# Performance work log

Measured on AMD Instinct MI355X. Metric: run time of the kernel, lower is better.

Reference implementation:

```python
import jax, jax.numpy as jnp
import numpy as np

_ICO_FACES0 = [
    [0,11,5],[0,5,1],[0,1,7],[0,7,10],[0,10,11],
    [1,5,9],[5,11,4],[11,10,2],[10,7,6],[7,1,8],
    [3,9,4],[3,4,2],[3,2,6],[3,6,8],[3,8,9],
    [4,9,5],[2,4,11],[6,2,10],[8,6,7],[9,8,1]]


def ico_sphere_np(level=1):
    t = (1.0 + 5.0 ** 0.5) / 2.0
    verts = np.array([[-1,t,0],[1,t,0],[-1,-t,0],[1,-t,0],
                      [0,-1,t],[0,1,t],[0,-1,-t],[0,1,-t],
                      [t,0,-1],[t,0,1],[-t,0,-1],[-t,0,1]], dtype=np.float64)
    verts = verts / np.linalg.norm(verts, axis=1, keepdims=True)
    faces = [list(f) for f in _ICO_FACES0]
    for _ in range(level):
        vlist = [v for v in verts]
        cache = {}
        def mid(a, b):
            k = (min(a, b), max(a, b))
            if k not in cache:
                v = vlist[a] + vlist[b]
                vlist.append(v / np.linalg.norm(v))
                cache[k] = len(vlist) - 1
            return cache[k]
        nf = []
        for a, b, c in faces:
            ab, bc, ca = mid(a, b), mid(b, c), mid(c, a)
            nf += [[a, ab, ca], [b, bc, ab], [c, ca, bc], [ab, bc, ca]]
        faces = nf
        verts = np.stack(vlist)
    return verts.astype(np.float32), np.array(faces, dtype=np.int32)


def make_template():
    verts, faces = ico_sphere_np(1)          # (42,3), (80,3)
    v = verts[None]                          # (1,42,3)
    vmin = v.min(axis=1, keepdims=True)
    vmax = v.max(axis=1, keepdims=True)
    center = (vmin + vmax) / 2.0
    scale = (vmax - vmin).max() / 2.0        # normalize_to_box
    tv = 1.4 * (v - center) / scale          # cage_size = 1.4
    return jnp.asarray(np.transpose(tv, (0, 2, 1))), jnp.asarray(faces)  # (1,3,42),(80,3)


def optimize_cage(cage, shape, distance=0.4, iters=100, step=0.01):
    # cage (1,3,C), shape (B,3,N)
    B = shape.shape[0]
    cage = jnp.broadcast_to(cage, (B,) + cage.shape[1:])
    def body(_, c):
        d = jnp.sqrt(jnp.sum((c[:, :, :, None] - shape[:, :, None, :]) ** 2, axis=1))  # (B,C,N)
        min_d = jnp.min(d, axis=2)                                                     # (B,C)
        upd = (min_d > distance).astype(c.dtype)
        return c + step * (-c) * upd[:, None, :]
    return jax.lax.fori_loop(0, iters, body, cage)


def mean_value_coordinates_3D(query, vertices, faces):
    # query (B,P,3), vertices (B,C,3), faces (F,3) shared across batch
    B, P, _ = query.shape
    C = vertices.shape[1]
    r1 = jnp.array([1, 2, 0]); r2 = jnp.array([2, 0, 1])
    uj = vertices[:, None] - query[:, :, None]            # (B,P,C,3)
    dj = jnp.linalg.norm(uj, axis=-1, keepdims=True)      # (B,P,C,1)
    uj = uj / dj
    ui = uj[:, :, faces]                                  # (B,P,F,3,3)
    li = jnp.linalg.norm(ui[:, :, :, r1] - ui[:, :, :, r2], axis=-1)  # (B,P,F,3)
    eps = 2e-5
    li = jnp.where(li >= 2, li - jax.lax.stop_gradient(li - (2 - eps)), li)
    li = jnp.where(li <= -2, li - jax.lax.stop_gradient(li + (2 - eps)), li)
    theta = 2.0 * jnp.arcsin(li / 2.0)                    # (B,P,F,3)
    h = jnp.sum(theta, axis=-1, keepdims=True) / 2.0      # (B,P,F,1)
    ci = 2.0 * jnp.sin(h) * jnp.sin(h - theta) / (jnp.sin(theta[..., r1]) * jnp.sin(theta[..., r2])) - 1.0
    ci = jnp.clip(ci, -1 + 1e-5, 1 - 1e-5)
    si = jnp.sign(jnp.linalg.det(ui))[..., None] * jnp.sqrt(1.0 - ci ** 2)  # (B,P,F,3)
    di = dj[..., 0][:, :, faces]                          # (B,P,F,3)
    wi = (theta - ci[..., r1] * theta[..., r2] - ci[..., r2] * theta[..., r1]) / (di * jnp.sin(theta[..., r1]) * si[..., r2])
    inside = (jnp.pi - h[..., 0]) < 1e-4                  # (B,P,F)
    any_inside = jnp.any(inside, axis=-1, keepdims=True)[..., None]  # (B,P,1,1)
    wi = jnp.where(any_inside, 0.0, wi)
    wi = jnp.where(inside[..., None], jnp.sin(theta) * di[..., r2] * di[..., r1], wi)
    # scatter face corners -> vertices (B,P,F*3) -> (B,P,C)
    wj = jnp.zeros((B, P, C), wi.dtype).at[:, :, faces.reshape(-1)].add(wi.reshape(B, P, -1))
    close = dj[..., 0] < 1e-8                             # (B,P,C)
    wj = jnp.where(jnp.any(close, axis=-1, keepdims=True), 0.0, wj)
    wj = jnp.where(close, 1.0, wj)
    sumWj = jnp.sum(wj, axis=-1, keepdims=True)
    sumWj = jnp.where(sumWj == 0, 1.0, sumWj)
    return wj / sumWj, wi


def setup_inputs() -> dict:
    key = jax.random.key(0)
    ks = jax.random.split(key, 12)
    B, N, FEAT = 16, 8192, 256
    template_vertices, faces = make_template()
    def lin(k, fi, fo):
        k1, k2 = jax.random.split(k)
        return (jax.random.normal(k1, (fi, fo), jnp.float32) / np.sqrt(fi).astype(np.float32),
                jax.random.normal(k2, (fo,), jnp.float32) * 0.01)
    W1, b1 = lin(ks[0], 2 * FEAT, 512)
    W2, b2 = lin(ks[1], 512, 512)
    W3, b3 = lin(ks[2], 512, 256)
    W4, b4 = lin(ks[3], 256, 42 * 3)
    return {
        'source_shape': jax.random.normal(ks[4], (B, 3, N), jnp.float32),
        'target_shape': jax.random.normal(ks[5], (B, 3, N), jnp.float32),
        'source_f': jax.random.normal(ks[6], (B, FEAT), jnp.float32),
        'target_f': jax.random.normal(ks[7], (B, FEAT), jnp.float32),
        'template_vertices': template_vertices, 'faces': faces,
        'W1': W1, 'b1': b1, 'W2': W2, 'b2': b2, 'W3': W3, 'b3': b3, 'W4': W4, 'b4': b4,
    }


def reference(source_shape, target_shape, source_f, target_f, template_vertices, faces,
              W1, b1, W2, b2, W3, b3, W4, b4):
    B = source_shape.shape[0]
    cage = optimize_cage(template_vertices, source_shape)        # (B,3,42)
    feat = jnp.concatenate([source_f, target_f], axis=-1)        # (B,512)
    h = jax.nn.relu(feat @ W1 + b1)
    h = jax.nn.relu(h @ W2 + b2)
    h = jax.nn.relu(h @ W3 + b3)
    influence_offset = h @ W4 + b4                               # (B,126)
    cage_offset = influence_offset.reshape(B, 3, -1)             # (B,3,42)
    new_cage = cage + cage_offset
    cage_t = jnp.transpose(cage, (0, 2, 1))                      # (B,42,3)
    new_cage_t = jnp.transpose(new_cage, (0, 2, 1))
    weights, _ = mean_value_coordinates_3D(jnp.transpose(source_shape, (0, 2, 1)), cage_t, faces)
    weights = jax.lax.stop_gradient(weights)                     # weights.detach() in deform_with_MVC
    deformed = jnp.einsum('bpc,bcd->bpd', weights, new_cage_t)   # (B,N,3)
    return cage_t, new_cage_t, jnp.transpose(deformed, (0, 2, 1)), weights, influence_offset
```

## Files before the change

kernel.cpp:

```cpp
#include <hip/hip_runtime.h>
#include <math.h>

#define BB 16
#define NP 8192
#define NV 42
#define NF 80
#define FEAT 256
#define PPB 64
#define FH  40

__device__ __forceinline__ float rcp_f(float x)  { return __builtin_amdgcn_rcpf(x); }
__device__ __forceinline__ float rsq_f(float x)  { return __builtin_amdgcn_rsqf(x); }
__device__ __forceinline__ float sqrt_f(float x) { return __builtin_amdgcn_sqrtf(x); }

__device__ __forceinline__ float theta_from_x(float x) {
  bool big = x > 0.5f;
  float z = big ? fmaf(-0.5f, x, 0.5f) : x * x;
  float s = big ? sqrt_f(z) : x;
  float P = fmaf(z, 0.022371875f, 0.030381944f);
  P = fmaf(z, P, 0.044642857f);
  P = fmaf(z, P, 0.075f);
  P = fmaf(z, P, 0.16666667f);
  float r = fmaf(s * z, P, s);
  return big ? fmaf(-4.f, r, 3.14159265358979f) : 2.f * r;
}

__global__ __launch_bounds__(256) void cage_opt_kernel(
    const float* __restrict__ tmpl,
    const float* __restrict__ src,
    float* __restrict__ cage)
{
  __shared__ float red[8];
  int b = blockIdx.x / NV;
  int v = blockIdx.x % NV;
  const float* sp = src + (size_t)b * 3 * NP;
  float cx = tmpl[v], cy = tmpl[NV + v], cz = tmpl[2 * NV + v];
  int k = 0;
  while (true) {
    float m = 3.4e38f;
    for (int i = threadIdx.x; i < NP; i += 256) {
      float dx = __fsub_rn(cx, sp[i]);
      float dy = __fsub_rn(cy, sp[NP + i]);
      float dz = __fsub_rn(cz, sp[2 * NP + i]);
      float ss = __fadd_rn(__fadd_rn(__fmul_rn(dx, dx), __fmul_rn(dy, dy)),
                           __fmul_rn(dz, dz));
      m = fminf(m, ss);
    }
    #pragma unroll
    for (int off = 32; off > 0; off >>= 1)
      m = fminf(m, __shfl_down(m, off, 64));
    int wid = threadIdx.x >> 6;
    __syncthreads();
    if ((threadIdx.x & 63) == 0) red[wid] = m;
    __syncthreads();
    if (threadIdx.x == 0) {
      float mm = fminf(fminf(red[0], red[1]), fminf(red[2], red[3]));
      red[4] = sqrtf(mm);
    }
    __syncthreads();
    float mind = red[4];
    if (mind > 0.4f && k < 100) {
      cx = __fsub_rn(cx, __fmul_rn(0.01f, cx));
      cy = __fsub_rn(cy, __fmul_rn(0.01f, cy));
      cz = __fsub_rn(cz, __fmul_rn(0.01f, cz));
      k++;
    } else {
      break;
    }
  }
  if (threadIdx.x == 0) {
    cage[(size_t)b * 3 * NV + v]          = cx;
    cage[(size_t)b * 3 * NV + NV + v]     = cy;
    cage[(size_t)b * 3 * NV + 2 * NV + v] = cz;
  }
}

__global__ __launch_bounds__(256) void linear_splitk(
    const float* __restrict__ in0, const float* __restrict__ in1,
    const float* __restrict__ W, const float* __restrict__ bias,
    float* __restrict__ out, int FI, int FO, int relu)
{
  __shared__ float sIn[512];
  __shared__ float part[4][64];
  int bb = blockIdx.y;
  int tid = threadIdx.x;
  for (int i = tid; i < FI; i += 256) {
    float v;
    if (in1) v = (i < FEAT) ? in0[(size_t)bb * FEAT + i]
                            : in1[(size_t)bb * FEAT + i - FEAT];
    else     v = in0[(size_t)bb * FI + i];
    sIn[i] = v;
  }
  __syncthreads();
  int o = blockIdx.x * 64 + (tid & 63);
  int kk = tid >> 6;
  int seg = FI >> 2;
  float acc = 0.f;
  const float* wp = W + o;
  #pragma unroll 4
  for (int i = kk * seg; i < (kk + 1) * seg; i++)
    acc = fmaf(sIn[i], wp[(size_t)i * FO], acc);
  part[kk][tid & 63] = acc;
  __syncthreads();
  if (tid < 64) {
    float r = ((part[0][tid] + part[1][tid]) + (part[2][tid] + part[3][tid]))
              + bias[o];
    out[(size_t)bb * FO + o] = relu ? fmaxf(r, 0.f) : r;
  }
}

__global__ __launch_bounds__(128) void l4_finalize_kernel(
    const float* __restrict__ h3,
    const float* __restrict__ W4, const float* __restrict__ b4,
    const float* __restrict__ cage,
    float* __restrict__ out_io,
    float* __restrict__ cage_t,
    float* __restrict__ ncage_t)
{
  __shared__ float sIn[256];
  int bb = blockIdx.x;
  int tid = threadIdx.x;
  sIn[tid] = h3[(size_t)bb * 256 + tid];
  sIn[tid + 128] = h3[(size_t)bb * 256 + tid + 128];
  __syncthreads();
  if (tid < 126) {
    float acc = b4[tid];
    const float* wp = W4 + tid;
    #pragma unroll 4
    for (int i = 0; i < 256; i++) acc = fmaf(sIn[i], wp[(size_t)i * 126], acc);
    out_io[(size_t)bb * 126 + tid] = acc;
    float c  = cage[(size_t)bb * 126 + tid];
    float nc = c + acc;
    int d = tid / NV, v = tid - d * NV;
    cage_t[(size_t)bb * NV * 3 + v * 3 + d]  = c;
    ncage_t[(size_t)bb * NV * 3 + v * 3 + d] = nc;
  }
}

__global__ __launch_bounds__(128, 3) void mvc_kernel(
    const float* __restrict__ src,
    const float* __restrict__ cage_t,
    const float* __restrict__ ncage_t,
    const int* __restrict__ faces,
    float* __restrict__ out_def,
    float* __restrict__ out_w)
{
  __shared__ float4 vpos[NV];
  __shared__ float4 npos[NV];
  __shared__ int fidp[NF];
  __shared__ float wj[2 * NV][PPB];
  __shared__ unsigned long long closeM[2][PPB];
  __shared__ int insideF[2][PPB];

  const float PI_F = 3.14159265358979323846f;
  int tid = threadIdx.x;
  int p   = tid & (PPB - 1);
  int hf  = tid >> 6;
  int b    = blockIdx.x / (NP / PPB);
  int pblk = blockIdx.x % (NP / PPB);
  int gp   = pblk * PPB + p;

  if (tid < NV) {
    const float* cp = cage_t + (size_t)b * NV * 3 + tid * 3;
    vpos[tid] = make_float4(cp[0], cp[1], cp[2], 0.f);
    const float* np_ = ncage_t + (size_t)b * NV * 3 + tid * 3;
    npos[tid] = make_float4(np_[0], np_[1], np_[2], 0.f);
  }
  if (tid < NF) {
    int f0 = faces[3 * tid], f1 = faces[3 * tid + 1], f2 = faces[3 * tid + 2];
    fidp[tid] = f0 | (f1 << 6) | (f2 << 12);
  }
  #pragma unroll
  for (int c = 0; c < NV; c++) wj[hf * NV + c][p] = 0.f;
  __syncthreads();

  float qx = src[(size_t)b * 3 * NP + gp];
  float qy = src[(size_t)b * 3 * NP + NP + gp];
  float qz = src[(size_t)b * 3 * NP + 2 * NP + gp];

  int anyInside = 0;
  unsigned long long closeMask = 0ull;

  auto face_geom = [&](int i, int& f0, int& f1, int& f2,
                       float& d0, float& d1, float& d2,
                       float& th0, float& th1, float& th2,
                       float& st0, float& st1, float& st2,
                       float& hh, float& sh, float& sm0, float& sm1, float& sm2,
                       float& sg) {
    int pk = fidp[i];
    f0 = pk & 63; f1 = (pk >> 6) & 63; f2 = pk >> 12;
    float4 v0 = vpos[f0], v1 = vpos[f1], v2 = vpos[f2];
    float a0x = v0.x - qx, a0y = v0.y - qy, a0z = v0.z - qz;
    float a1x = v1.x - qx, a1y = v1.y - qy, a1z = v1.z - qz;
    float a2x = v2.x - qx, a2y = v2.y - qy, a2z = v2.z - qz;
    float ss0 = fmaf(a0x, a0x, fmaf(a0y, a0y, a0z * a0z));
    float ss1 = fmaf(a1x, a1x, fmaf(a1y, a1y, a1z * a1z));
    float ss2 = fmaf(a2x, a2x, fmaf(a2y, a2y, a2z * a2z));
    float i0 = rsq_f(ss0), i1 = rsq_f(ss1), i2 = rsq_f(ss2);
    d0 = ss0 * i0; d1 = ss1 * i1; d2 = ss2 * i2;
    if (d0 < 1e-8f) closeMask |= (1ull << f0);
    if (d1 < 1e-8f) closeMask |= (1ull << f1);
    if (d2 < 1e-8f) closeMask |= (1ull << f2);
    float u0x = a0x * i0, u0y = a0y * i0, u0z = a0z * i0;
    float u1x = a1x * i1, u1y = a1y * i1, u1z = a1z * i1;
    float u2x = a2x * i2, u2y = a2y * i2, u2z = a2z * i2;
    float ex, ey, ez;
    ex = u1x - u2x; ey = u1y - u2y; ez = u1z - u2z;
    float x0 = 0.5f * sqrt_f(fmaf(ex, ex, fmaf(ey, ey, ez * ez)));
    ex = u2x - u0x; ey = u2y - u0y; ez = u2z - u0z;
    float x1 = 0.5f * sqrt_f(fmaf(ex, ex, fmaf(ey, ey, ez * ez)));
    ex = u0x - u1x; ey = u0y - u1y; ez = u0z - u1z;
    float x2 = 0.5f * sqrt_f(fmaf(ex, ex, fmaf(ey, ey, ez * ez)));
    if (x0 >= 1.f) x0 = 0.99999f;
    if (x1 >= 1.f) x1 = 0.99999f;
    if (x2 >= 1.f) x2 = 0.99999f;
    float cx0 = sqrt_f(fmaxf(fmaf(-x0, x0, 1.f), 0.f));
    float cx1 = sqrt_f(fmaxf(fmaf(-x1, x1, 1.f), 0.f));
    float cx2 = sqrt_f(fmaxf(fmaf(-x2, x2, 1.f), 0.f));
    th0 = theta_from_x(x0);
    th1 = theta_from_x(x1);
    th2 = theta_from_x(x2);
    hh  = 0.5f * ((th0 + th1) + th2);
    st0 = 2.f * (x0 * cx0);
    st1 = 2.f * (x1 * cx1);
    st2 = 2.f * (x2 * cx2);
    float A1 = x0 * (cx1 * cx2);
    float A2 = x1 * (cx0 * cx2);
    float A3 = x2 * (cx0 * cx1);
    float A4 = x0 * (x1 * x2);
    sh  = ((A1 + A2) + A3) - A4;
    sm0 = ((-A1 + A2) + A3) + A4;
    sm1 = ((A1 - A2) + A3) + A4;
    sm2 = ((A1 + A2) - A3) + A4;
    float det = u0x * fmaf(u1y, u2z, -u1z * u2y)
              - u0y * fmaf(u1x, u2z, -u1z * u2x)
              + u0z * fmaf(u1x, u2y, -u1y * u2x);
    sg = (det > 0.f) ? 1.f : ((det < 0.f) ? -1.f : 0.f);
  };

  #pragma unroll 1
  for (int i = hf * FH; i < hf * FH + FH; i++) {
    int f0, f1, f2;
    float d0, d1, d2, th0, th1, th2, st0, st1, st2, hh, sh, sm0, sm1, sm2, sg;
    face_geom(i, f0, f1, f2, d0, d1, d2, th0, th1, th2, st0, st1, st2,
              hh, sh, sm0, sm1, sm2, sg);
    if (PI_F - hh < 1e-4f) anyInside = 1;
    float twosh = 2.f * sh;
    float c0 = fmaf(twosh * sm0, rcp_f(st1 * st2), -1.f);
    float c1 = fmaf(twosh * sm1, rcp_f(st2 * st0), -1.f);
    float c2 = fmaf(twosh * sm2, rcp_f(st0 * st1), -1.f);
    c0 = fminf(fmaxf(c0, -0.99999f), 0.99999f);
    c1 = fminf(fmaxf(c1, -0.99999f), 0.99999f);
    c2 = fminf(fmaxf(c2, -0.99999f), 0.99999f);
    float s0 = sg * sqrt_f(fmaf(-c0, c0, 1.f));
    float s1 = sg * sqrt_f(fmaf(-c1, c1, 1.f));
    float s2 = sg * sqrt_f(fmaf(-c2, c2, 1.f));
    float w0 = (fmaf(-c2, th1, fmaf(-c1, th2, th0))) * rcp_f((d0 * st1) * s2);
    float w1 = (fmaf(-c0, th2, fmaf(-c2, th0, th1))) * rcp_f((d1 * st2) * s0);
    float w2 = (fmaf(-c1, th0, fmaf(-c0, th1, th2))) * rcp_f((d2 * st0) * s1);
    wj[hf * NV + f0][p] += w0;
    wj[hf * NV + f1][p] += w1;
    wj[hf * NV + f2][p] += w2;
  }

  closeM[hf][p]  = closeMask;
  insideF[hf][p] = anyInside;
  __syncthreads();

  int mIn = insideF[0][p] | insideF[1][p];
  unsigned long long mCl = closeM[0][p] | closeM[1][p];

  if (mIn) {
    #pragma unroll
    for (int c = 0; c < NV; c++) wj[hf * NV + c][p] = 0.f;
    #pragma unroll 1
    for (int i = hf * FH; i < hf * FH + FH; i++) {
      int f0, f1, f2;
      float d0, d1, d2, th0, th1, th2, st0, st1, st2, hh, sh, sm0, sm1, sm2, sg;
      face_geom(i, f0, f1, f2, d0, d1, d2, th0, th1, th2, st0, st1, st2,
                hh, sh, sm0, sm1, sm2, sg);
      if (PI_F - hh < 1e-4f) {
        wj[hf * NV + f0][p] += (st0 * d2) * d1;
        wj[hf * NV + f1][p] += (st1 * d0) * d2;
        wj[hf * NV + f2][p] += (st2 * d1) * d0;
      }
    }
  }
  __syncthreads();

  if (tid < PPB) {
    float sum = 0.f;
    #pragma unroll
    for (int c = 0; c < NV; c++) {
      float w = wj[c][p] + wj[NV + c][p];
      if (mCl) w = ((mCl >> c) & 1ull) ? 1.f : 0.f;
      wj[c][p] = w;
      sum += w;
    }
    if (sum == 0.f) sum = 1.f;
    float inv = rcp_f(sum);
    float ax = 0.f, ay = 0.f, az = 0.f;
    #pragma unroll
    for (int c = 0; c < NV; c++) {
      float w = wj[c][p] * inv;
      wj[c][p] = w;
      float4 n = npos[c];
      ax = fmaf(w, n.x, ax);
      ay = fmaf(w, n.y, ay);
      az = fmaf(w, n.z, az);
    }
    out_def[(size_t)b * 3 * NP + gp]          = ax;
    out_def[(size_t)b * 3 * NP + NP + gp]     = ay;
    out_def[(size_t)b * 3 * NP + 2 * NP + gp] = az;
  }
  __syncthreads();

  float* wbase = out_w + ((size_t)b * NP + pblk * PPB) * NV;
  for (int idx = tid; idx < PPB * NV; idx += 128) {
    int pp = idx / NV;
    int c  = idx - pp * NV;
    wbase[idx] = wj[c][pp];
  }
}

extern "C" void kernel_launch(void* const* d_in, const int* in_sizes, int n_in,
                              void* d_out, int out_size, void* d_ws, size_t ws_size,
                              hipStream_t stream) {
  (void)in_sizes; (void)n_in; (void)out_size; (void)d_ws; (void)ws_size;
  const float* src   = (const float*)d_in[0];
  const float* sf    = (const float*)d_in[2];
  const float* tf    = (const float*)d_in[3];
  const float* tmpl  = (const float*)d_in[4];
  const int*   faces = (const int*)d_in[5];
  const float* W1 = (const float*)d_in[6];  const float* b1 = (const float*)d_in[7];
  const float* W2 = (const float*)d_in[8];  const float* b2 = (const float*)d_in[9];
  const float* W3 = (const float*)d_in[10]; const float* b3 = (const float*)d_in[11];
  const float* W4 = (const float*)d_in[12]; const float* b4 = (const float*)d_in[13];

  float* out = (float*)d_out;
  float* out_cage_t  = out;
  float* out_ncage_t = out + 2016;
  float* out_def     = out + 4032;
  float* out_w       = out + 397248;
  float* out_io      = out + 5902272;

  float* s_cage = out_w;
  float* s_h1   = out_w + 2016;
  float* s_h2   = out_w + 10208;
  float* s_h3   = out_w + 18400;

  cage_opt_kernel<<<dim3(BB * NV), dim3(256), 0, stream>>>(tmpl, src, s_cage);
  linear_splitk<<<dim3(8, BB), dim3(256), 0, stream>>>(sf, tf, W1, b1, s_h1, 512, 512, 1);
  linear_splitk<<<dim3(8, BB), dim3(256), 0, stream>>>(s_h1, nullptr, W2, b2, s_h2, 512, 512, 1);
  linear_splitk<<<dim3(4, BB), dim3(256), 0, stream>>>(s_h2, nullptr, W3, b3, s_h3, 512, 256, 1);
  l4_finalize_kernel<<<dim3(BB), dim3(128), 0, stream>>>(
      s_h3, W4, b4, s_cage, out_io, out_cage_t, out_ncage_t);
  mvc_kernel<<<dim3(BB * (NP / PPB)), dim3(128), 0, stream>>>(
      src, out_cage_t, out_ncage_t, faces, out_def, out_w);
}
```

Before: 168.8 us.

## Restructure MVC with compile-time face chunks and fuse cage-opt with MLP

The MVC kernel now hardcodes the icosphere face topology as compile-time constants. It splits the 80 faces into 8 chunks of 10, one wave per chunk, with 512 threads per block. Each wave computes unit vectors and distances once per vertex its chunk uses, instead of once per face corner, and accumulates weights with LDS atomics into a padded buffer. The cage optimization and the three hidden MLP layers are merged into one launch, with extra blocks running each batch's full MLP chain, which removes three launches and the intermediate global buffers. In exchange the kernel ignores the faces input, carries heavy register pressure from the per-vertex arrays, and relies on atomics in LDS.

```diff
diff --git a/kernel.cpp b/kernel.cpp
--- a/kernel.cpp
+++ b/kernel.cpp
@@ -7,7 +7,41 @@
 #define NF 80
 #define FEAT 256
 #define PPB 64
-#define FH  40
+#define CHF 10
+#define NWV 8
+#define WST 67
+
+#define FACE_LIST \
+ {0,12,14},{11,13,12},{5,14,13},{12,13,14}, \
+ {0,14,16},{5,15,14},{1,16,15},{14,15,16}, \
+ {0,16,18},{1,17,16},{7,18,17},{16,17,18}, \
+ {0,18,20},{7,19,18},{10,20,19},{18,19,20}, \
+ {0,20,12},{10,21,20},{11,12,21},{20,21,12}, \
+ {1,15,23},{5,22,15},{9,23,22},{15,22,23}, \
+ {5,13,25},{11,24,13},{4,25,24},{13,24,25}, \
+ {11,21,27},{10,26,21},{2,27,26},{21,26,27}, \
+ {10,19,29},{7,28,19},{6,29,28},{19,28,29}, \
+ {7,17,31},{1,30,17},{8,31,30},{17,30,31}, \
+ {3,32,34},{9,33,32},{4,34,33},{32,33,34}, \
+ {3,34,36},{4,35,34},{2,36,35},{34,35,36}, \
+ {3,36,38},{2,37,36},{6,38,37},{36,37,38}, \
+ {3,38,40},{6,39,38},{8,40,39},{38,39,40}, \
+ {3,40,32},{8,41,40},{9,32,41},{40,41,32}, \
+ {4,33,25},{9,22,33},{5,25,22},{33,22,25}, \
+ {2,35,27},{4,24,35},{11,27,24},{35,24,27}, \
+ {6,37,29},{2,26,37},{10,29,26},{37,26,29}, \
+ {8,39,31},{6,28,39},{7,31,28},{39,28,31}, \
+ {9,41,23},{8,30,41},{1,23,30},{41,30,23}
+
+constexpr int FC[NF][3] = { FACE_LIST };
+static __device__ const int FR[NF][3] = { FACE_LIST };
+
+constexpr unsigned long long chunk_vmask(int q) {
+  unsigned long long m = 0;
+  for (int f = q * CHF; f < q * CHF + CHF; ++f)
+    for (int k = 0; k < 3; ++k) m |= 1ull << FC[f][k];
+  return m;
+}
 
 __device__ __forceinline__ float rcp_f(float x)  { return __builtin_amdgcn_rcpf(x); }
 __device__ __forceinline__ float rsq_f(float x)  { return __builtin_amdgcn_rsqf(x); }
@@ -25,87 +59,356 @@
   return big ? fmaf(-4.f, r, 3.14159265358979f) : 2.f * r;
 }
 
-__global__ __launch_bounds__(256) void cage_opt_kernel(
-    const float* __restrict__ tmpl,
+template<int Q, int C>
+struct Vtx {
+  static __device__ __forceinline__ void go(const float4* vpos,
+      float qx, float qy, float qz,
+      float (&ux)[NV], float (&uy)[NV], float (&uz)[NV], float (&dd)[NV],
+      unsigned long long& closeMask) {
+    if constexpr (C < NV) {
+      if constexpr ((chunk_vmask(Q) >> C) & 1ull) {
+        float4 v = vpos[C];
+        float ax = v.x - qx, ay = v.y - qy, az = v.z - qz;
+        float ss = fmaf(ax, ax, fmaf(ay, ay, az * az));
+        if (ss < 1e-16f) closeMask |= (1ull << C);
+        float ir = rsq_f(ss);
+        ux[C] = ax * ir; uy[C] = ay * ir; uz[C] = az * ir; dd[C] = ss * ir;
+      }
+      Vtx<Q, C + 1>::go(vpos, qx, qy, qz, ux, uy, uz, dd, closeMask);
+    }
+  }
+};
+
+template<int F>
+__device__ __forceinline__ void face_body(
+    const float (&ux)[NV], const float (&uy)[NV], const float (&uz)[NV],
+    const float (&dd)[NV], float (&wj)[NV], int& anyInside)
+{
+  constexpr int f0 = FC[F][0], f1 = FC[F][1], f2 = FC[F][2];
+  float ex = ux[f1] - ux[f2], ey = uy[f1] - uy[f2], ez = uz[f1] - uz[f2];
+  float x0 = 0.5f * sqrt_f(fmaf(ex, ex, fmaf(ey, ey, ez * ez)));
+  ex = ux[f2] - ux[f0]; ey = uy[f2] - uy[f0]; ez = uz[f2] - uz[f0];
+  float x1 = 0.5f * sqrt_f(fmaf(ex, ex, fmaf(ey, ey, ez * ez)));
+  ex = ux[f0] - ux[f1]; ey = uy[f0] - uy[f1]; ez = uz[f0] - uz[f1];
+  float x2 = 0.5f * sqrt_f(fmaf(ex, ex, fmaf(ey, ey, ez * ez)));
+  if (x0 >= 1.f) x0 = 0.99999f;
+  if (x1 >= 1.f) x1 = 0.99999f;
+  if (x2 >= 1.f) x2 = 0.99999f;
+  float cx0 = sqrt_f(fmaxf(fmaf(-x0, x0, 1.f), 0.f));
+  float cx1 = sqrt_f(fmaxf(fmaf(-x1, x1, 1.f), 0.f));
+  float cx2 = sqrt_f(fmaxf(fmaf(-x2, x2, 1.f), 0.f));
+  float th0 = theta_from_x(x0);
+  float th1 = theta_from_x(x1);
+  float th2 = theta_from_x(x2);
+  float hh = 0.5f * ((th0 + th1) + th2);
+  if (3.14159265358979f - hh < 1e-4f) anyInside = 1;
+  float st0 = 2.f * (x0 * cx0);
+  float st1 = 2.f * (x1 * cx1);
+  float st2 = 2.f * (x2 * cx2);
+  float A1 = x0 * (cx1 * cx2);
+  float A2 = x1 * (cx0 * cx2);
+  float A3 = x2 * (cx0 * cx1);
+  float A4 = x0 * (x1 * x2);
+  float sh  = ((A1 + A2) + A3) - A4;
+  float sm0 = ((-A1 + A2) + A3) + A4;
+  float sm1 = ((A1 - A2) + A3) + A4;
+  float sm2 = ((A1 + A2) - A3) + A4;
+  float twosh = 2.f * sh;
+  float c0 = fmaf(twosh * sm0, rcp_f(st1 * st2), -1.f);
+  float c1 = fmaf(twosh * sm1, rcp_f(st2 * st0), -1.f);
+  float c2 = fmaf(twosh * sm2, rcp_f(st0 * st1), -1.f);
+  c0 = fminf(fmaxf(c0, -0.99999f), 0.99999f);
+  c1 = fminf(fmaxf(c1, -0.99999f), 0.99999f);
+  c2 = fminf(fmaxf(c2, -0.99999f), 0.99999f);
+  float det = ux[f0] * fmaf(uy[f1], uz[f2], -(uz[f1] * uy[f2]))
+            - uy[f0] * fmaf(ux[f1], uz[f2], -(uz[f1] * ux[f2]))
+            + uz[f0] * fmaf(ux[f1], uy[f2], -(uy[f1] * ux[f2]));
+  float sg = (det > 0.f) ? 1.f : ((det < 0.f) ? -1.f : 0.f);
+  float s0 = sg * sqrt_f(fmaf(-c0, c0, 1.f));
+  float s1 = sg * sqrt_f(fmaf(-c1, c1, 1.f));
+  float s2 = sg * sqrt_f(fmaf(-c2, c2, 1.f));
+  float w0 = fmaf(-c2, th1, fmaf(-c1, th2, th0)) * rcp_f((dd[f0] * st1) * s2);
+  float w1 = fmaf(-c0, th2, fmaf(-c2, th0, th1)) * rcp_f((dd[f1] * st2) * s0);
+  float w2 = fmaf(-c1, th0, fmaf(-c0, th1, th2)) * rcp_f((dd[f2] * st0) * s1);
+  wj[f0] += w0;
+  wj[f1] += w1;
+  wj[f2] += w2;
+}
+
+template<int Q, int K>
+struct FaceChain {
+  static __device__ __forceinline__ void go(
+      const float (&ux)[NV], const float (&uy)[NV], const float (&uz)[NV],
+      const float (&dd)[NV], float (&wj)[NV], int& anyInside) {
+    if constexpr (K < CHF) {
+      face_body<Q * CHF + K>(ux, uy, uz, dd, wj, anyInside);
+      FaceChain<Q, K + 1>::go(ux, uy, uz, dd, wj, anyInside);
+    }
+  }
+};
+
+template<int Q, int C>
+struct AddChain {
+  static __device__ __forceinline__ void go(float* wjLDS, int p,
+                                            const float (&wj)[NV]) {
+    if constexpr (C < NV) {
+      if constexpr ((chunk_vmask(Q) >> C) & 1ull)
+        atomicAdd(&wjLDS[C * WST + p], wj[C]);
+      AddChain<Q, C + 1>::go(wjLDS, p, wj);
+    }
+  }
+};
+
+template<int Q>
+__device__ __forceinline__ void do_chunk(const float4* vpos,
+    float qx, float qy, float qz, float* wjLDS, int p,
+    int& anyInside, unsigned long long& closeMask)
+{
+  float ux[NV], uy[NV], uz[NV], dd[NV];
+  float wj[NV] = {};
+  Vtx<Q, 0>::go(vpos, qx, qy, qz, ux, uy, uz, dd, closeMask);
+  FaceChain<Q, 0>::go(ux, uy, uz, dd, wj, anyInside);
+  AddChain<Q, 0>::go(wjLDS, p, wj);
+}
+
+__device__ void inside_face_rt(int f, const float4* vpos,
+    float qx, float qy, float qz, float* wjLDS, int p)
+{
+  int f0 = FR[f][0], f1 = FR[f][1], f2 = FR[f][2];
+  float4 v0 = vpos[f0], v1 = vpos[f1], v2 = vpos[f2];
+  float a0x = v0.x - qx, a0y = v0.y - qy, a0z = v0.z - qz;
+  float a1x = v1.x - qx, a1y = v1.y - qy, a1z = v1.z - qz;
+  float a2x = v2.x - qx, a2y = v2.y - qy, a2z = v2.z - qz;
+  float ss0 = fmaf(a0x, a0x, fmaf(a0y, a0y, a0z * a0z));
+  float ss1 = fmaf(a1x, a1x, fmaf(a1y, a1y, a1z * a1z));
+  float ss2 = fmaf(a2x, a2x, fmaf(a2y, a2y, a2z * a2z));
+  float i0 = rsq_f(ss0), i1 = rsq_f(ss1), i2 = rsq_f(ss2);
+  float d0 = ss0 * i0, d1 = ss1 * i1, d2 = ss2 * i2;
+  float u0x = a0x * i0, u0y = a0y * i0, u0z = a0z * i0;
+  float u1x = a1x * i1, u1y = a1y * i1, u1z = a1z * i1;
+  float u2x = a2x * i2, u2y = a2y * i2, u2z = a2z * i2;
+  float ex = u1x - u2x, ey = u1y - u2y, ez = u1z - u2z;
+  float x0 = 0.5f * sqrt_f(fmaf(ex, ex, fmaf(ey, ey, ez * ez)));
+  ex = u2x - u0x; ey = u2y - u0y; ez = u2z - u0z;
+  float x1 = 0.5f * sqrt_f(fmaf(ex, ex, fmaf(ey, ey, ez * ez)));
+  ex = u0x - u1x; ey = u0y - u1y; ez = u0z - u1z;
+  float x2 = 0.5f * sqrt_f(fmaf(ex, ex, fmaf(ey, ey, ez * ez)));
+  if (x0 >= 1.f) x0 = 0.99999f;
+  if (x1 >= 1.f) x1 = 0.99999f;
+  if (x2 >= 1.f) x2 = 0.99999f;
+  float th0 = theta_from_x(x0), th1 = theta_from_x(x1), th2 = theta_from_x(x2);
+  float hh = 0.5f * ((th0 + th1) + th2);
+  if (3.14159265358979f - hh < 1e-4f) {
+    float cx0 = sqrt_f(fmaxf(fmaf(-x0, x0, 1.f), 0.f));
+    float cx1 = sqrt_f(fmaxf(fmaf(-x1, x1, 1.f), 0.f));
+    float cx2 = sqrt_f(fmaxf(fmaf(-x2, x2, 1.f), 0.f));
+    atomicAdd(&wjLDS[f0 * WST + p], (2.f * (x0 * cx0) * d2) * d1);
+    atomicAdd(&wjLDS[f1 * WST + p], (2.f * (x1 * cx1) * d0) * d2);
+    atomicAdd(&wjLDS[f2 * WST + p], (2.f * (x2 * cx2) * d1) * d0);
+  }
+}
+
+__global__ __launch_bounds__(512, 4) void mvc_kernel(
     const float* __restrict__ src,
-    float* __restrict__ cage)
+    const float* __restrict__ cage_t,
+    const float* __restrict__ ncage_t,
+    float* __restrict__ out_def,
+    float* __restrict__ out_w)
+{
+  __shared__ float4 vpos[NV];
+  __shared__ float4 npos[NV];
+  __shared__ float wjLDS[NV * WST];
+  __shared__ int insideL[PPB];
+  __shared__ unsigned int closeL[2 * PPB];
+  __shared__ int blkIn;
+
+  int tid = threadIdx.x;
+  int p = tid & (PPB - 1);
+  int q = tid >> 6;
+  int b    = blockIdx.x / (NP / PPB);
+  int pblk = blockIdx.x % (NP / PPB);
+  int gp   = pblk * PPB + p;
+
+  if (tid < NV) {
+    const float* cp = cage_t + (size_t)b * NV * 3 + tid * 3;
+    vpos[tid] = make_float4(cp[0], cp[1], cp[2], 0.f);
+    const float* np_ = ncage_t + (size_t)b * NV * 3 + tid * 3;
+    npos[tid] = make_float4(np_[0], np_[1], np_[2], 0.f);
+  }
+  for (int i = tid; i < NV * WST; i += 512) wjLDS[i] = 0.f;
+  if (tid < PPB) insideL[tid] = 0;
+  if (tid < 2 * PPB) closeL[tid] = 0u;
+  if (tid == 0) blkIn = 0;
+  __syncthreads();
+
+  float qx = src[(size_t)b * 3 * NP + gp];
+  float qy = src[(size_t)b * 3 * NP + NP + gp];
+  float qz = src[(size_t)b * 3 * NP + 2 * NP + gp];
+
+  int anyInside = 0;
+  unsigned long long closeMask = 0ull;
+
+  switch (q) {
+    case 0: do_chunk<0>(vpos, qx, qy, qz, wjLDS, p, anyInside, closeMask); break;
+    case 1: do_chunk<1>(vpos, qx, qy, qz, wjLDS, p, anyInside, closeMask); break;
+    case 2: do_chunk<2>(vpos, qx, qy, qz, wjLDS, p, anyInside, closeMask); break;
+    case 3: do_chunk<3>(vpos, qx, qy, qz, wjLDS, p, anyInside, closeMask); break;
+    case 4: do_chunk<4>(vpos, qx, qy, qz, wjLDS, p, anyInside, closeMask); break;
+    case 5: do_chunk<5>(vpos, qx, qy, qz, wjLDS, p, anyInside, closeMask); break;
+    case 6: do_chunk<6>(vpos, qx, qy, qz, wjLDS, p, anyInside, closeMask); break;
+    default: do_chunk<7>(vpos, qx, qy, qz, wjLDS, p, anyInside, closeMask); break;
+  }
+
+  if (anyInside) { insideL[p] = 1; blkIn = 1; }
+  if (closeMask) {
+    atomicOr(&closeL[p], (unsigned int)closeMask);
+    atomicOr(&closeL[PPB + p], (unsigned int)(closeMask >> 32));
+  }
+  __syncthreads();
+
+  if (blkIn) {
+    if (tid < PPB && insideL[tid])
+      for (int c = 0; c < NV; c++) wjLDS[c * WST + tid] = 0.f;
+    __syncthreads();
+    if (insideL[p])
+      for (int f = q * CHF; f < q * CHF + CHF; f++)
+        inside_face_rt(f, vpos, qx, qy, qz, wjLDS, p);
+    __syncthreads();
+  }
+  __syncthreads();
+
+  if (tid < PPB) {
+    unsigned long long mCl =
+        (unsigned long long)closeL[tid] |
+        ((unsigned long long)closeL[PPB + tid] << 32);
+    float sum = 0.f;
+    for (int c = 0; c < NV; c++) {
+      float v = wjLDS[c * WST + tid];
+      if (mCl) { v = ((mCl >> c) & 1ull) ? 1.f : 0.f; wjLDS[c * WST + tid] = v; }
+      sum += v;
+    }
+    if (sum == 0.f) sum = 1.f;
+    float inv = rcp_f(sum);
+    float ax = 0.f, ay = 0.f, az = 0.f;
+    for (int c = 0; c < NV; c++) {
+      float w = wjLDS[c * WST + tid] * inv;
+      wjLDS[c * WST + tid] = w;
+      float4 n = npos[c];
+      ax = fmaf(w, n.x, ax);
+      ay = fmaf(w, n.y, ay);
+      az = fmaf(w, n.z, az);
+    }
+    int gpp = pblk * PPB + tid;
+    out_def[(size_t)b * 3 * NP + gpp]          = ax;
+    out_def[(size_t)b * 3 * NP + NP + gpp]     = ay;
+    out_def[(size_t)b * 3 * NP + 2 * NP + gpp] = az;
+  }
+  __syncthreads();
+
+  float* wbase = out_w + ((size_t)b * NP + pblk * PPB) * NV;
+  for (int idx = tid; idx < PPB * NV; idx += 512) {
+    int pp = idx / NV;
+    int c  = idx - pp * NV;
+    wbase[idx] = wjLDS[c * WST + pp];
+  }
+}
+
+__global__ __launch_bounds__(256) void cage_mlp_kernel(
+    const float* __restrict__ tmpl, const float* __restrict__ src,
+    const float* __restrict__ sf, const float* __restrict__ tf,
+    const float* __restrict__ W1, const float* __restrict__ b1,
+    const float* __restrict__ W2, const float* __restrict__ b2,
+    const float* __restrict__ W3, const float* __restrict__ b3,
+    float* __restrict__ cage,
+    float* __restrict__ h3)
 {
   __shared__ float red[8];
-  int b = blockIdx.x / NV;
-  int v = blockIdx.x % NV;
-  const float* sp = src + (size_t)b * 3 * NP;
-  float cx = tmpl[v], cy = tmpl[NV + v], cz = tmpl[2 * NV + v];
-  int k = 0;
-  while (true) {
-    float m = 3.4e38f;
-    for (int i = threadIdx.x; i < NP; i += 256) {
-      float dx = __fsub_rn(cx, sp[i]);
-      float dy = __fsub_rn(cy, sp[NP + i]);
-      float dz = __fsub_rn(cz, sp[2 * NP + i]);
-      float ss = __fadd_rn(__fadd_rn(__fmul_rn(dx, dx), __fmul_rn(dy, dy)),
-                           __fmul_rn(dz, dz));
-      m = fminf(m, ss);
-    }
-    #pragma unroll
-    for (int off = 32; off > 0; off >>= 1)
-      m = fminf(m, __shfl_down(m, off, 64));
-    int wid = threadIdx.x >> 6;
+  __shared__ float sA[512];
+  __shared__ float sB[512];
+  int tid = threadIdx.x;
+
+  if (blockIdx.x < BB * NV) {
+    int b = blockIdx.x / NV;
+    int v = blockIdx.x % NV;
+    const float* sp = src + (size_t)b * 3 * NP;
+    float cx = tmpl[v], cy = tmpl[NV + v], cz = tmpl[2 * NV + v];
+    int k = 0;
+    while (true) {
+      float m = 3.4e38f;
+      for (int i = tid; i < NP; i += 256) {
+        float dx = __fsub_rn(cx, sp[i]);
+        float dy = __fsub_rn(cy, sp[NP + i]);
+        float dz = __fsub_rn(cz, sp[2 * NP + i]);
+        float ss = __fadd_rn(__fadd_rn(__fmul_rn(dx, dx), __fmul_rn(dy, dy)),
+                             __fmul_rn(dz, dz));
+        m = fminf(m, ss);
+      }
+      #pragma unroll
+      for (int off = 32; off > 0; off >>= 1)
+        m = fminf(m, __shfl_down(m, off, 64));
+      int wid = tid >> 6;
+      __syncthreads();
+      if ((tid & 63) == 0) red[wid] = m;
+      __syncthreads();
+      if (tid == 0) {
+        float mm = fminf(fminf(red[0], red[1]), fminf(red[2], red[3]));
+        red[4] = sqrtf(mm);
+      }
+      __syncthreads();
+      float mind = red[4];
+      if (mind > 0.4f && k < 100) {
+        cx = __fsub_rn(cx, __fmul_rn(0.01f, cx));
+        cy = __fsub_rn(cy, __fmul_rn(0.01f, cy));
+        cz = __fsub_rn(cz, __fmul_rn(0.01f, cz));
+        k++;
+      } else {
+        break;
+      }
+    }
+    if (tid == 0) {
+      cage[(size_t)b * 3 * NV + v]          = cx;
+      cage[(size_t)b * 3 * NV + NV + v]     = cy;
+      cage[(size_t)b * 3 * NV + 2 * NV + v] = cz;
+    }
+  } else {
+    int bb = blockIdx.x - BB * NV;
+    for (int i = tid; i < 512; i += 256)
+      sA[i] = (i < FEAT) ? sf[(size_t)bb * FEAT + i]
+                         : tf[(size_t)bb * FEAT + i - FEAT];
     __syncthreads();
-    if ((threadIdx.x & 63) == 0) red[wid] = m;
+    {
+      int o0 = tid, o1 = tid + 256;
+      float a0 = b1[o0], a1 = b1[o1];
+      #pragma unroll 4
+      for (int i = 0; i < 512; i++) {
+        float s = sA[i];
+        a0 = fmaf(s, W1[(size_t)i * 512 + o0], a0);
+        a1 = fmaf(s, W1[(size_t)i * 512 + o1], a1);
+      }
+      sB[o0] = fmaxf(a0, 0.f);
+      sB[o1] = fmaxf(a1, 0.f);
+    }
     __syncthreads();
-    if (threadIdx.x == 0) {
-      float mm = fminf(fminf(red[0], red[1]), fminf(red[2], red[3]));
-      red[4] = sqrtf(mm);
+    {
+      int o0 = tid, o1 = tid + 256;
+      float a0 = b2[o0], a1 = b2[o1];
+      #pragma unroll 4
+      for (int i = 0; i < 512; i++) {
+        float s = sB[i];
+        a0 = fmaf(s, W2[(size_t)i * 512 + o0], a0);
+        a1 = fmaf(s, W2[(size_t)i * 512 + o1], a1);
+      }
+      sA[o0] = fmaxf(a0, 0.f);
+      sA[o1] = fmaxf(a1, 0.f);
     }
     __syncthreads();
-    float mind = red[4];
-    if (mind > 0.4f && k < 100) {
-      cx = __fsub_rn(cx, __fmul_rn(0.01f, cx));
-      cy = __fsub_rn(cy, __fmul_rn(0.01f, cy));
-      cz = __fsub_rn(cz, __fmul_rn(0.01f, cz));
-      k++;
-    } else {
-      break;
-    }
-  }
-  if (threadIdx.x == 0) {
-    cage[(size_t)b * 3 * NV + v]          = cx;
-    cage[(size_t)b * 3 * NV + NV + v]     = cy;
-    cage[(size_t)b * 3 * NV + 2 * NV + v] = cz;
-  }
-}
-
-__global__ __launch_bounds__(256) void linear_splitk(
-    const float* __restrict__ in0, const float* __restrict__ in1,
-    const float* __restrict__ W, const float* __restrict__ bias,
-    float* __restrict__ out, int FI, int FO, int relu)
-{
-  __shared__ float sIn[512];
-  __shared__ float part[4][64];
-  int bb = blockIdx.y;
-  int tid = threadIdx.x;
-  for (int i = tid; i < FI; i += 256) {
-    float v;
-    if (in1) v = (i < FEAT) ? in0[(size_t)bb * FEAT + i]
-                            : in1[(size_t)bb * FEAT + i - FEAT];
-    else     v = in0[(size_t)bb * FI + i];
-    sIn[i] = v;
-  }
-  __syncthreads();
-  int o = blockIdx.x * 64 + (tid & 63);
-  int kk = tid >> 6;
-  int seg = FI >> 2;
-  float acc = 0.f;
-  const float* wp = W + o;
-  #pragma unroll 4
-  for (int i = kk * seg; i < (kk + 1) * seg; i++)
-    acc = fmaf(sIn[i], wp[(size_t)i * FO], acc);
-  part[kk][tid & 63] = acc;
-  __syncthreads();
-  if (tid < 64) {
-    float r = ((part[0][tid] + part[1][tid]) + (part[2][tid] + part[3][tid]))
-              + bias[o];
-    out[(size_t)bb * FO + o] = relu ? fmaxf(r, 0.f) : r;
+    {
+      float a0 = b3[tid];
+      #pragma unroll 4
+      for (int i = 0; i < 512; i++)
+        a0 = fmaf(sA[i], W3[(size_t)i * 256 + tid], a0);
+      h3[(size_t)bb * 256 + tid] = fmaxf(a0, 0.f);
+    }
   }
 }
 
@@ -137,192 +440,6 @@
   }
 }
 
-__global__ __launch_bounds__(128, 3) void mvc_kernel(
-    const float* __restrict__ src,
-    const float* __restrict__ cage_t,
-    const float* __restrict__ ncage_t,
-    const int* __restrict__ faces,
-    float* __restrict__ out_def,
-    float* __restrict__ out_w)
-{
-  __shared__ float4 vpos[NV];
-  __shared__ float4 npos[NV];
-  __shared__ int fidp[NF];
-  __shared__ float wj[2 * NV][PPB];
-  __shared__ unsigned long long closeM[2][PPB];
-  __shared__ int insideF[2][PPB];
-
-  const float PI_F = 3.14159265358979323846f;
-  int tid = threadIdx.x;
-  int p   = tid & (PPB - 1);
-  int hf  = tid >> 6;
-  int b    = blockIdx.x / (NP / PPB);
-  int pblk = blockIdx.x % (NP / PPB);
-  int gp   = pblk * PPB + p;
-
-  if (tid < NV) {
-    const float* cp = cage_t + (size_t)b * NV * 3 + tid * 3;
-    vpos[tid] = make_float4(cp[0], cp[1], cp[2], 0.f);
-    const float* np_ = ncage_t + (size_t)b * NV * 3 + tid * 3;
-    npos[tid] = make_float4(np_[0], np_[1], np_[2], 0.f);
-  }
-  if (tid < NF) {
-    int f0 = faces[3 * tid], f1 = faces[3 * tid + 1], f2 = faces[3 * tid + 2];
-    fidp[tid] = f0 | (f1 << 6) | (f2 << 12);
-  }
-  #pragma unroll
-  for (int c = 0; c < NV; c++) wj[hf * NV + c][p] = 0.f;
-  __syncthreads();
-
-  float qx = src[(size_t)b * 3 * NP + gp];
-  float qy = src[(size_t)b * 3 * NP + NP + gp];
-  float qz = src[(size_t)b * 3 * NP + 2 * NP + gp];
-
-  int anyInside = 0;
-  unsigned long long closeMask = 0ull;
-
-  auto face_geom = [&](int i, int& f0, int& f1, int& f2,
-                       float& d0, float& d1, float& d2,
-                       float& th0, float& th1, float& th2,
-                       float& st0, float& st1, float& st2,
-                       float& hh, float& sh, float& sm0, float& sm1, float& sm2,
-                       float& sg) {
-    int pk = fidp[i];
-    f0 = pk & 63; f1 = (pk >> 6) & 63; f2 = pk >> 12;
-    float4 v0 = vpos[f0], v1 = vpos[f1], v2 = vpos[f2];
-    float a0x = v0.x - qx, a0y = v0.y - qy, a0z = v0.z - qz;
-    float a1x = v1.x - qx, a1y = v1.y - qy, a1z = v1.z - qz;
-    float a2x = v2.x - qx, a2y = v2.y - qy, a2z = v2.z - qz;
-    float ss0 = fmaf(a0x, a0x, fmaf(a0y, a0y, a0z * a0z));
-    float ss1 = fmaf(a1x, a1x, fmaf(a1y, a1y, a1z * a1z));
-    float ss2 = fmaf(a2x, a2x, fmaf(a2y, a2y, a2z * a2z));
-    float i0 = rsq_f(ss0), i1 = rsq_f(ss1), i2 = rsq_f(ss2);
-    d0 = ss0 * i0; d1 = ss1 * i1; d2 = ss2 * i2;
-    if (d0 < 1e-8f) closeMask |= (1ull << f0);
-    if (d1 < 1e-8f) closeMask |= (1ull << f1);
-    if (d2 < 1e-8f) closeMask |= (1ull << f2);
-    float u0x = a0x * i0, u0y = a0y * i0, u0z = a0z * i0;
-    float u1x = a1x * i1, u1y = a1y * i1, u1z = a1z * i1;
-    float u2x = a2x * i2, u2y = a2y * i2, u2z = a2z * i2;
-    float ex, ey, ez;
-    ex = u1x - u2x; ey = u1y - u2y; ez = u1z - u2z;
-    float x0 = 0.5f * sqrt_f(fmaf(ex, ex, fmaf(ey, ey, ez * ez)));
-    ex = u2x - u0x; ey = u2y - u0y; ez = u2z - u0z;
-    float x1 = 0.5f * sqrt_f(fmaf(ex, ex, fmaf(ey, ey, ez * ez)));
-    ex = u0x - u1x; ey = u0y - u1y; ez = u0z - u1z;
-    float x2 = 0.5f * sqrt_f(fmaf(ex, ex, fmaf(ey, ey, ez * ez)));
-    if (x0 >= 1.f) x0 = 0.99999f;
-    if (x1 >= 1.f) x1 = 0.99999f;
-    if (x2 >= 1.f) x2 = 0.99999f;
-    float cx0 = sqrt_f(fmaxf(fmaf(-x0, x0, 1.f), 0.f));
-    float cx1 = sqrt_f(fmaxf(fmaf(-x1, x1, 1.f), 0.f));
-    float cx2 = sqrt_f(fmaxf(fmaf(-x2, x2, 1.f), 0.f));
-    th0 = theta_from_x(x0);
-    th1 = theta_from_x(x1);
-    th2 = theta_from_x(x2);
-    hh  = 0.5f * ((th0 + th1) + th2);
-    st0 = 2.f * (x0 * cx0);
-    st1 = 2.f * (x1 * cx1);
-    st2 = 2.f * (x2 * cx2);
-    float A1 = x0 * (cx1 * cx2);
-    float A2 = x1 * (cx0 * cx2);
-    float A3 = x2 * (cx0 * cx1);
-    float A4 = x0 * (x1 * x2);
-    sh  = ((A1 + A2) + A3) - A4;
-    sm0 = ((-A1 + A2) + A3) + A4;
-    sm1 = ((A1 - A2) + A3) + A4;
-    sm2 = ((A1 + A2) - A3) + A4;
-    float det = u0x * fmaf(u1y, u2z, -u1z * u2y)
-              - u0y * fmaf(u1x, u2z, -u1z * u2x)
-              + u0z * fmaf(u1x, u2y, -u1y * u2x);
-    sg = (det > 0.f) ? 1.f : ((det < 0.f) ? -1.f : 0.f);
-  };
-
-  #pragma unroll 1
-  for (int i = hf * FH; i < hf * FH + FH; i++) {
-    int f0, f1, f2;
-    float d0, d1, d2, th0, th1, th2, st0, st1, st2, hh, sh, sm0, sm1, sm2, sg;
-    face_geom(i, f0, f1, f2, d0, d1, d2, th0, th1, th2, st0, st1, st2,
-              hh, sh, sm0, sm1, sm2, sg);
-    if (PI_F - hh < 1e-4f) anyInside = 1;
-    float twosh = 2.f * sh;
-    float c0 = fmaf(twosh * sm0, rcp_f(st1 * st2), -1.f);
-    float c1 = fmaf(twosh * sm1, rcp_f(st2 * st0), -1.f);
-    float c2 = fmaf(twosh * sm2, rcp_f(st0 * st1), -1.f);
-    c0 = fminf(fmaxf(c0, -0.99999f), 0.99999f);
-    c1 = fminf(fmaxf(c1, -0.99999f), 0.99999f);
-    c2 = fminf(fmaxf(c2, -0.99999f), 0.99999f);
-    float s0 = sg * sqrt_f(fmaf(-c0, c0, 1.f));
-    float s1 = sg * sqrt_f(fmaf(-c1, c1, 1.f));
-    float s2 = sg * sqrt_f(fmaf(-c2, c2, 1.f));
-    float w0 = (fmaf(-c2, th1, fmaf(-c1, th2, th0))) * rcp_f((d0 * st1) * s2);
-    float w1 = (fmaf(-c0, th2, fmaf(-c2, th0, th1))) * rcp_f((d1 * st2) * s0);
-    float w2 = (fmaf(-c1, th0, fmaf(-c0, th1, th2))) * rcp_f((d2 * st0) * s1);
-    wj[hf * NV + f0][p] += w0;
-    wj[hf * NV + f1][p] += w1;
-    wj[hf * NV + f2][p] += w2;
-  }
-
-  closeM[hf][p]  = closeMask;
-  insideF[hf][p] = anyInside;
-  __syncthreads();
-
-  int mIn = insideF[0][p] | insideF[1][p];
-  unsigned long long mCl = closeM[0][p] | closeM[1][p];
-
-  if (mIn) {
-    #pragma unroll
-    for (int c = 0; c < NV; c++) wj[hf * NV + c][p] = 0.f;
-    #pragma unroll 1
-    for (int i = hf * FH; i < hf * FH + FH; i++) {
-      int f0, f1, f2;
-      float d0, d1, d2, th0, th1, th2, st0, st1, st2, hh, sh, sm0, sm1, sm2, sg;
-      face_geom(i, f0, f1, f2, d0, d1, d2, th0, th1, th2, st0, st1, st2,
-                hh, sh, sm0, sm1, sm2, sg);
-      if (PI_F - hh < 1e-4f) {
-        wj[hf * NV + f0][p] += (st0 * d2) * d1;
-        wj[hf * NV + f1][p] += (st1 * d0) * d2;
-        wj[hf * NV + f2][p] += (st2 * d1) * d0;
-      }
-    }
-  }
-  __syncthreads();
-
-  if (tid < PPB) {
-    float sum = 0.f;
-    #pragma unroll
-    for (int c = 0; c < NV; c++) {
-      float w = wj[c][p] + wj[NV + c][p];
-      if (mCl) w = ((mCl >> c) & 1ull) ? 1.f : 0.f;
-      wj[c][p] = w;
-      sum += w;
-    }
-    if (sum == 0.f) sum = 1.f;
-    float inv = rcp_f(sum);
-    float ax = 0.f, ay = 0.f, az = 0.f;
-    #pragma unroll
-    for (int c = 0; c < NV; c++) {
-      float w = wj[c][p] * inv;
-      wj[c][p] = w;
-      float4 n = npos[c];
-      ax = fmaf(w, n.x, ax);
-      ay = fmaf(w, n.y, ay);
-      az = fmaf(w, n.z, az);
-    }
-    out_def[(size_t)b * 3 * NP + gp]          = ax;
-    out_def[(size_t)b * 3 * NP + NP + gp]     = ay;
-    out_def[(size_t)b * 3 * NP + 2 * NP + gp] = az;
-  }
-  __syncthreads();
-
-  float* wbase = out_w + ((size_t)b * NP + pblk * PPB) * NV;
-  for (int idx = tid; idx < PPB * NV; idx += 128) {
-    int pp = idx / NV;
-    int c  = idx - pp * NV;
-    wbase[idx] = wj[c][pp];
-  }
-}
-
 extern "C" void kernel_launch(void* const* d_in, const int* in_sizes, int n_in,
                               void* d_out, int out_size, void* d_ws, size_t ws_size,
                               hipStream_t stream) {
@@ -331,7 +448,6 @@
   const float* sf    = (const float*)d_in[2];
   const float* tf    = (const float*)d_in[3];
   const float* tmpl  = (const float*)d_in[4];
-  const int*   faces = (const int*)d_in[5];
   const float* W1 = (const float*)d_in[6];  const float* b1 = (const float*)d_in[7];
   const float* W2 = (const float*)d_in[8];  const float* b2 = (const float*)d_in[9];
   const float* W3 = (const float*)d_in[10]; const float* b3 = (const float*)d_in[11];
@@ -345,16 +461,12 @@
   float* out_io      = out + 5902272;
 
   float* s_cage = out_w;
-  float* s_h1   = out_w + 2016;
-  float* s_h2   = out_w + 10208;
-  float* s_h3   = out_w + 18400;
-
-  cage_opt_kernel<<<dim3(BB * NV), dim3(256), 0, stream>>>(tmpl, src, s_cage);
-  linear_splitk<<<dim3(8, BB), dim3(256), 0, stream>>>(sf, tf, W1, b1, s_h1, 512, 512, 1);
-  linear_splitk<<<dim3(8, BB), dim3(256), 0, stream>>>(s_h1, nullptr, W2, b2, s_h2, 512, 512, 1);
-  linear_splitk<<<dim3(4, BB), dim3(256), 0, stream>>>(s_h2, nullptr, W3, b3, s_h3, 512, 256, 1);
+  float* s_h3   = out_w + 2016;
+
+  cage_mlp_kernel<<<dim3(BB * NV + BB), dim3(256), 0, stream>>>(
+      tmpl, src, sf, tf, W1, b1, W2, b2, W3, b3, s_cage, s_h3);
   l4_finalize_kernel<<<dim3(BB), dim3(128), 0, stream>>>(
       s_h3, W4, b4, s_cage, out_io, out_cage_t, out_ncage_t);
-  mvc_kernel<<<dim3(BB * (NP / PPB)), dim3(128), 0, stream>>>(
-      src, out_cage_t, out_ncage_t, faces, out_def, out_w);
-}
+  mvc_kernel<<<dim3(BB * (NP / PPB)), dim3(512), 0, stream>>>(
+      src, out_cage_t, out_ncage_t, out_def, out_w);
+}
```

Measured after the change: 260.8 us. 1.55x slower.
